# Performance work log

Measured on AMD Instinct MI355X. Metric: run time of the kernel, lower is better.

The kernel has to match this reference:

```python
import jax, jax.numpy as jnp
import numpy as np

TEMPERATURE = 0.5


def setup_inputs() -> dict:
    key = jax.random.key(0)
    ks = jax.random.split(key, 12)
    B, N, T = 128, 64, 256
    IN, H, OUT = N + T, 256, 128
    E = N * (N - 1) // 2  # 2016 upper-tri edges per graph
    total_edges = B * E
    inp = {
        "x_topology": jax.random.normal(ks[0], (B, N, N), jnp.float32),
        "x_temporal": jax.random.normal(ks[1], (B, N, T), jnp.float32),
        "gumbel_u": jax.random.uniform(ks[2], (total_edges,), jnp.float32, 1e-6, 1.0),
        # GNNLayer linear
        "W_gnn": jax.random.normal(ks[3], (IN, H), jnp.float32) / np.sqrt(IN),
        "b_gnn": jnp.zeros((H,), jnp.float32),
        # edge heads (input dim 2*H)
        "W_mean": jax.random.normal(ks[4], (2 * H, OUT), jnp.float32) / np.sqrt(2 * H),
        "b_mean": jnp.zeros((OUT,), jnp.float32),
        "W_var": jax.random.normal(ks[5], (2 * H, OUT), jnp.float32) / np.sqrt(2 * H),
        "b_var": jnp.zeros((OUT,), jnp.float32),
        "W_w": jax.random.normal(ks[6], (2 * H, 1), jnp.float32) / np.sqrt(2 * H),
        "b_w": jnp.zeros((1,), jnp.float32),
    }
    return inp


def reference(x_topology, x_temporal, gumbel_u, W_gnn, b_gnn,
              W_mean, b_mean, W_var, b_var, W_w, b_w):
    B, N, _ = x_topology.shape
    T = x_temporal.shape[-1]
    # Upper-triangular fully-connected edge index (no self loops), batched with node offsets.
    row, col = jnp.triu_indices(N, k=1)          # [E]
    E = row.shape[0]
    offs = (jnp.arange(B) * N)[:, None]          # [B,1]
    src = (row[None, :] + offs).reshape(-1)       # [B*E]
    dst = (col[None, :] + offs).reshape(-1)       # [B*E]

    # Node features: concat topology + temporal, flatten batch of graphs.
    x = jnp.concatenate([x_topology, x_temporal], axis=-1).reshape(B * N, N + T)

    # Mean aggregation (PyG aggr='mean'): messages x[src] scattered to dst; 0 for isolated nodes.
    msg_sum = jax.ops.segment_sum(x[src], dst, num_segments=B * N)      # [B*N, N+T]
    cnt = jax.ops.segment_sum(jnp.ones_like(src, x.dtype), dst, num_segments=B * N)
    agg = jnp.where(cnt[:, None] > 0, msg_sum / jnp.maximum(cnt, 1.0)[:, None], 0.0)

    h = jax.nn.relu(agg @ W_gnn + b_gnn)          # [B*N, H]

    # Edge MLP heads on gathered [src||dst] embeddings.
    ef = jnp.concatenate([h[src], h[dst]], axis=-1)        # [B*E, 2H]
    mean = ef @ W_mean + b_mean                             # [B*E, OUT]
    variance = jax.nn.softplus(ef @ W_var + b_var) + 1e-6   # [B*E, OUT]
    weight = jax.nn.sigmoid((ef @ W_w + b_w)[:, 0])          # [B*E]

    # Gumbel-softmax over the flattened edge-weight vector (dim=-1 of a 1-D tensor).
    g = -jnp.log(-jnp.log(gumbel_u))
    gumbel_w = jax.nn.softmax((weight + g) / TEMPERATURE, axis=-1)

    # Gaussian similarity per edge, scatter into dense adjacency.
    sim = jnp.exp(-0.5 * jnp.mean(mean ** 2 / (variance + 1e-8), axis=-1))
    edge_w = sim * gumbel_w                                  # [B*E]

    b_idx = jnp.repeat(jnp.arange(B), E)
    adj = jnp.zeros((B, N, N), x.dtype).at[b_idx, jnp.tile(row, B), jnp.tile(col, B)].set(edge_w)
    return adj
```

## Files before the change

kernel.cpp:

```cpp
#include <hip/hip_runtime.h>
#include <hip/hip_bf16.h>
#include <math.h>

#define Bg   128
#define Nn   64
#define Tt   256
#define INF  320
#define Hd   256
#define OUTD 128
#define Ee   2016
#define TOTE (Bg*Ee)
#define SCOLS 576
#define MROWS 8192

typedef __attribute__((ext_vector_type(8))) short bf16x8;
typedef __attribute__((ext_vector_type(4))) float f32x4;

static __device__ __forceinline__ ushort f2bf(float v) {
    __hip_bfloat16 h = __float2bfloat16(v);
    return *(ushort*)&h;
}
static __device__ __forceinline__ unsigned fkey(float x) {
    unsigned b = __float_as_uint(x);
    return (b & 0x80000000u) ? ~b : (b | 0x80000000u);
}
static __device__ __forceinline__ float fkeyinv(unsigned k) {
    unsigned b = (k & 0x80000000u) ? (k ^ 0x80000000u) : ~k;
    return __uint_as_float(b);
}

#define CVT_N (INF * Hd)
#define PACK_N (Hd * SCOLS)
__global__ void k_prep(const float* __restrict__ Wg, const float* __restrict__ Wm,
                       const float* __restrict__ Wv, const float* __restrict__ Ww,
                       const float* __restrict__ bm, const float* __restrict__ bv,
                       const float* __restrict__ bw,
                       ushort* __restrict__ Wgb, ushort* __restrict__ Wcat,
                       float* __restrict__ ebias, unsigned* __restrict__ red) {
    int idx = blockIdx.x * 256 + threadIdx.x;
    if (idx == 0) { red[0] = 0u; red[1] = 0u; }
    if (idx < CVT_N) {
        Wgb[idx] = f2bf(Wg[idx]);
        return;
    }
    idx -= CVT_N;
    if (idx < PACK_N) {
        int k = idx / SCOLS, col = idx - k * SCOLS;
        float v = 0.f;
        if (col < 128)       v = Wm[k * 128 + col];
        else if (col < 256)  v = Wm[(256 + k) * 128 + (col - 128)];
        else if (col < 384)  v = Wv[k * 128 + (col - 256)];
        else if (col < 512)  v = Wv[(256 + k) * 128 + (col - 384)];
        else if (col == 512) v = Ww[k];
        else if (col == 513) v = Ww[256 + k];
        Wcat[idx] = f2bf(v);
        return;
    }
    idx -= PACK_N;
    if (idx >= SCOLS) return;
    float e = 0.f;
    if (idx < 128)                    e = bm[idx];
    else if (idx >= 256 && idx < 384) e = bv[idx - 256];
    else if (idx == 512)              e = bw[0];
    ebias[idx] = e;
}

__global__ __launch_bounds__(256) void k_agg(const float* __restrict__ topo,
                                             const float* __restrict__ temp,
                                             ushort* __restrict__ agg) {
    __shared__ float Ltr[64][5];
    int b = blockIdx.x;
    int w = threadIdx.x >> 6, lane = threadIdx.x & 63;
    int f = blockIdx.y * 4 + w;
    float x = (f < Nn) ? topo[(size_t)(b * Nn + lane) * Nn + f]
                       : temp[(size_t)(b * Nn + lane) * Tt + (f - Nn)];
    float incl = x;
    #pragma unroll
    for (int o = 1; o < 64; o <<= 1) {
        float t = __shfl_up(incl, o);
        if (lane >= o) incl += t;
    }
    float excl = incl - x;
    Ltr[lane][w] = lane ? excl / (float)lane : 0.f;
    __syncthreads();
    int node = threadIdx.x >> 2, fi = threadIdx.x & 3;
    agg[(size_t)(b * Nn + node) * INF + blockIdx.y * 4 + fi] = f2bf(Ltr[node][fi]);
}

__global__ __launch_bounds__(256) void k_gemm_mfma(const ushort* __restrict__ A,
                                                   const ushort* __restrict__ B,
                                                   const float* __restrict__ bias,
                                                   ushort* __restrict__ Cb,
                                                   float* __restrict__ Cf,
                                                   int N, int K, int relu, int transC) {
    __shared__ ushort Asl[64 * 32];
    __shared__ ushort Bsl[64 * 32];
    const int tid = threadIdx.x;
    const int w = tid >> 6, lane = tid & 63;
    const int quad = lane >> 4, r16 = lane & 15;
    const int m0 = blockIdx.y * 64, n0 = blockIdx.x * 64;
    const int arow = tid >> 2, aseg = tid & 3;
    const int bk = tid >> 3, bseg = tid & 7;
    f32x4 acc0 = {0,0,0,0}, acc1 = {0,0,0,0}, acc2 = {0,0,0,0}, acc3 = {0,0,0,0};

    for (int k0 = 0; k0 < K; k0 += 32) {
        uint4 av = *(const uint4*)(A + (size_t)(m0 + arow) * K + k0 + aseg * 8);
        *(uint4*)(Asl + arow * 32 + aseg * 8) = av;
        int bcol = n0 + bseg * 8;
        uint4 bvv = *(const uint4*)(B + (size_t)(k0 + bk) * N + bcol);
        ushort tmp[8];
        *(uint4*)tmp = bvv;
        #pragma unroll
        for (int t = 0; t < 8; ++t) Bsl[(bseg * 8 + t) * 32 + bk] = tmp[t];
        __syncthreads();

        bf16x8 af = *(const bf16x8*)(Asl + (w * 16 + r16) * 32 + quad * 8);
        bf16x8 bf0 = *(const bf16x8*)(Bsl + (0 * 16 + r16) * 32 + quad * 8);
        bf16x8 bf1 = *(const bf16x8*)(Bsl + (1 * 16 + r16) * 32 + quad * 8);
        bf16x8 bf2 = *(const bf16x8*)(Bsl + (2 * 16 + r16) * 32 + quad * 8);
        bf16x8 bf3 = *(const bf16x8*)(Bsl + (3 * 16 + r16) * 32 + quad * 8);
        acc0 = __builtin_amdgcn_mfma_f32_16x16x32_bf16(af, bf0, acc0, 0, 0, 0);
        acc1 = __builtin_amdgcn_mfma_f32_16x16x32_bf16(af, bf1, acc1, 0, 0, 0);
        acc2 = __builtin_amdgcn_mfma_f32_16x16x32_bf16(af, bf2, acc2, 0, 0, 0);
        acc3 = __builtin_amdgcn_mfma_f32_16x16x32_bf16(af, bf3, acc3, 0, 0, 0);
        __syncthreads();
    }

    const int row0 = m0 + w * 16 + quad * 4;
    #pragma unroll
    for (int ns = 0; ns < 4; ++ns) {
        f32x4 a = (ns == 0) ? acc0 : (ns == 1) ? acc1 : (ns == 2) ? acc2 : acc3;
        int col = n0 + ns * 16 + r16;
        float bb = bias ? bias[col] : 0.f;
        float vv[4];
        #pragma unroll
        for (int i = 0; i < 4; ++i) {
            float v = a[i] + bb;
            if (relu) v = fmaxf(v, 0.f);
            vv[i] = v;
        }
        if (transC) {
            *(float4*)(Cf + (size_t)col * MROWS + row0) = make_float4(vv[0], vv[1], vv[2], vv[3]);
        } else {
            #pragma unroll
            for (int i = 0; i < 4; ++i) {
                int row = row0 + i;
                if (Cb) Cb[(size_t)row * N + col] = f2bf(vv[i]);
                else    Cf[(size_t)row * N + col] = vv[i];
            }
        }
    }
}

static __device__ __forceinline__ float eterm(float pm, float qm, float pv, float qv) {
    float m = pm + qm;
    float x = pv + qv;
    float sp = fmaxf(x, 0.f) + __logf(1.f + __expf(-fabsf(x)));
    return m * m * __builtin_amdgcn_rcpf(sp + 1.01e-6f);
}

__global__ __launch_bounds__(256) void k_edge4(const float* __restrict__ ST,
                                               const float* __restrict__ gu,
                                               float* __restrict__ sim,
                                               float* __restrict__ lgt,
                                               unsigned* __restrict__ red) {
    __shared__ float L[4][16][132];
    __shared__ float sm[256];
    const int p = blockIdx.x % 10, b = blockIdx.x / 10;
    const int G0v[10] = {0,0,0,0,1,1,1,2,2,3};
    const int G1v[10] = {0,1,2,3,1,2,3,2,3,3};
    const int g0 = G0v[p], g1 = G1v[p];
    const int tid = threadIdx.x;

    #pragma unroll
    for (int rep = 0; rep < 8; ++rep) {
        int it = tid + 256 * rep;
        int arr = it >> 9;
        int c = (it >> 2) & 127, nq = it & 3;
        int g = (arr & 1) ? g1 : g0;
        float4 v = *(const float4*)&ST[(size_t)(arr * 128 + c) * MROWS + b * 64 + g * 16 + nq * 4];
        L[arr][nq * 4 + 0][c] = v.x;
        L[arr][nq * 4 + 1][c] = v.y;
        L[arr][nq * 4 + 2][c] = v.z;
        L[arr][nq * 4 + 3][c] = v.w;
    }
    __syncthreads();

    const int i = tid >> 4, j = tid & 15;
    float acc = 0.f;
    #pragma unroll 4
    for (int t = 0; t < 128; t += 4) {
        float4 mi = *(const float4*)&L[0][i][t];
        float4 mj = *(const float4*)&L[1][j][t];
        float4 vi = *(const float4*)&L[2][i][t];
        float4 vj = *(const float4*)&L[3][j][t];
        acc += eterm(mi.x, mj.x, vi.x, vj.x);
        acc += eterm(mi.y, mj.y, vi.y, vj.y);
        acc += eterm(mi.z, mj.z, vi.z, vj.z);
        acc += eterm(mi.w, mj.w, vi.w, vj.w);
    }

    const int ni = g0 * 16 + i, nj = g1 * 16 + j;
    float lv = -INFINITY;
    if (ni < nj) {
        int e = b * Ee + (ni * (127 - ni)) / 2 + (nj - ni - 1);
        float se = __expf(acc * (-1.f / 256.f));
        float wr = ST[(size_t)512 * MROWS + b * 64 + ni]
                 + ST[(size_t)513 * MROWS + b * 64 + nj];
        float w  = __builtin_amdgcn_rcpf(1.f + __expf(-wr));
        float g  = -__logf(-__logf(gu[e]));
        lv = (w + g) * 2.0f;
        sim[e] = se;
        lgt[e] = lv;
    }
    sm[tid] = lv; __syncthreads();
    for (int s = 128; s; s >>= 1) {
        if (tid < s) sm[tid] = fmaxf(sm[tid], sm[tid + s]);
        __syncthreads();
    }
    if (!tid) atomicMax(&red[0], fkey(sm[0]));
}

__global__ void k_red2(const float* __restrict__ lgt, unsigned* __restrict__ red) {
    __shared__ float sm[256];
    float M = fkeyinv(red[0]);
    float a = 0.f;
    for (int i = blockIdx.x * 256 + threadIdx.x; i < TOTE; i += 256 * 256)
        a += __expf(lgt[i] - M);
    sm[threadIdx.x] = a; __syncthreads();
    for (int s = 128; s; s >>= 1) {
        if (threadIdx.x < s) sm[threadIdx.x] += sm[threadIdx.x + s];
        __syncthreads();
    }
    if (!threadIdx.x) atomicAdd((float*)&red[1], sm[0]);
}

__global__ void k_out(const float* __restrict__ sim, const float* __restrict__ lgt,
                      const unsigned* __restrict__ red, float* __restrict__ out) {
    int idx = blockIdx.x * 256 + threadIdx.x;
    if (idx >= Bg * Nn * Nn) return;
    int b = idx >> 12;
    int rem = idx & 4095;
    int r = rem >> 6, c = rem & 63;
    float v = 0.f;
    if (c > r) {
        int e = b * Ee + (r * (127 - r)) / 2 + (c - r - 1);
        float M = fkeyinv(red[0]);
        float Sinv = __builtin_amdgcn_rcpf(__uint_as_float(red[1]));
        v = sim[e] * __expf(lgt[e] - M) * Sinv;
    }
    out[idx] = v;
}

extern "C" void kernel_launch(void* const* d_in, const int* in_sizes, int n_in,
                              void* d_out, int out_size, void* d_ws, size_t ws_size,
                              hipStream_t stream) {
    const float* topo = (const float*)d_in[0];
    const float* temp = (const float*)d_in[1];
    const float* gu   = (const float*)d_in[2];
    const float* Wg   = (const float*)d_in[3];
    const float* bg   = (const float*)d_in[4];
    const float* Wm   = (const float*)d_in[5];
    const float* bm   = (const float*)d_in[6];
    const float* Wv   = (const float*)d_in[7];
    const float* bv   = (const float*)d_in[8];
    const float* Ww   = (const float*)d_in[9];
    const float* bw   = (const float*)d_in[10];
    float* out = (float*)d_out;

    char* ws = (char*)d_ws;
    size_t off = 0;
    auto carve = [&](size_t bytes) { char* p = ws + off; off = (off + bytes + 255) & ~(size_t)255; return p; };

    char*   r1    = carve((size_t)SCOLS * MROWS * 4);
    float*  ST    = (float*)r1;
    ushort* aggb  = (ushort*)r1;
    ushort* hb    = (ushort*)carve((size_t)MROWS * Hd * 2);
    ushort* Wgb   = (ushort*)carve((size_t)INF * Hd * 2);
    ushort* Wcatb = (ushort*)carve((size_t)Hd * SCOLS * 2);
    float*  ebias = (float*)carve((size_t)SCOLS * 4);
    float*  sim   = (float*)carve((size_t)TOTE * 4);
    float*  lgt   = (float*)carve((size_t)TOTE * 4);
    unsigned* red = (unsigned*)carve(256);

    k_prep<<<(CVT_N + PACK_N + SCOLS + 255) / 256, 256, 0, stream>>>(
        Wg, Wm, Wv, Ww, bm, bv, bw, Wgb, Wcatb, ebias, red);
    k_agg<<<dim3(Bg, INF / 4), 256, 0, stream>>>(topo, temp, aggb);
    k_gemm_mfma<<<dim3(Hd / 64, MROWS / 64), 256, 0, stream>>>(
        aggb, Wgb, bg, hb, nullptr, Hd, INF, 1, 0);
    k_gemm_mfma<<<dim3(SCOLS / 64, MROWS / 64), 256, 0, stream>>>(
        hb, Wcatb, ebias, nullptr, ST, SCOLS, Hd, 0, 1);
    k_edge4<<<Bg * 10, 256, 0, stream>>>(ST, gu, sim, lgt, red);
    k_red2<<<256, 256, 0, stream>>>(lgt, red);
    k_out<<<(Bg * Nn * Nn + 255) / 256, 256, 0, stream>>>(sim, lgt, red, out);
}
```

Before: 162.0 us.

## Drop softmax max pass, transpose weights for GEMM, and batch aggregation tiles

Removes the max-reduction and the separate sum-reduction kernel. The edge kernel now computes exp of the logits directly, writes a single numerator buffer and atomically accumulates the denominator. Weights are stored pre-transposed so GEMM tiles load both operands with vector loads and a K=64 step, replacing scalar transposing LDS stores. The aggregation kernel handles 64 features per block via an LDS tile, with vectorized writes. Skipping the max subtraction relies on the logits being bounded, which risks overflow only for inputs outside that range.

Result: faster. 146.9 us (-9.3%).

```diff
diff --git a/kernel.cpp b/kernel.cpp
--- a/kernel.cpp
+++ b/kernel.cpp
@@ -20,14 +20,6 @@
     __hip_bfloat16 h = __float2bfloat16(v);
     return *(ushort*)&h;
 }
-static __device__ __forceinline__ unsigned fkey(float x) {
-    unsigned b = __float_as_uint(x);
-    return (b & 0x80000000u) ? ~b : (b | 0x80000000u);
-}
-static __device__ __forceinline__ float fkeyinv(unsigned k) {
-    unsigned b = (k & 0x80000000u) ? (k ^ 0x80000000u) : ~k;
-    return __uint_as_float(b);
-}
 
 #define CVT_N (INF * Hd)
 #define PACK_N (Hd * SCOLS)
@@ -35,25 +27,26 @@
                        const float* __restrict__ Wv, const float* __restrict__ Ww,
                        const float* __restrict__ bm, const float* __restrict__ bv,
                        const float* __restrict__ bw,
-                       ushort* __restrict__ Wgb, ushort* __restrict__ Wcat,
+                       ushort* __restrict__ WgbT, ushort* __restrict__ WcatT,
                        float* __restrict__ ebias, unsigned* __restrict__ red) {
     int idx = blockIdx.x * 256 + threadIdx.x;
     if (idx == 0) { red[0] = 0u; red[1] = 0u; }
     if (idx < CVT_N) {
-        Wgb[idx] = f2bf(Wg[idx]);
+        int n = idx / INF, k = idx - n * INF;
+        WgbT[idx] = f2bf(Wg[k * Hd + n]);
         return;
     }
     idx -= CVT_N;
     if (idx < PACK_N) {
-        int k = idx / SCOLS, col = idx - k * SCOLS;
+        int n = idx / Hd, k = idx - n * Hd;
         float v = 0.f;
-        if (col < 128)       v = Wm[k * 128 + col];
-        else if (col < 256)  v = Wm[(256 + k) * 128 + (col - 128)];
-        else if (col < 384)  v = Wv[k * 128 + (col - 256)];
-        else if (col < 512)  v = Wv[(256 + k) * 128 + (col - 384)];
-        else if (col == 512) v = Ww[k];
-        else if (col == 513) v = Ww[256 + k];
-        Wcat[idx] = f2bf(v);
+        if (n < 128)       v = Wm[k * 128 + n];
+        else if (n < 256)  v = Wm[(256 + k) * 128 + (n - 128)];
+        else if (n < 384)  v = Wv[k * 128 + (n - 256)];
+        else if (n < 512)  v = Wv[(256 + k) * 128 + (n - 384)];
+        else if (n == 512) v = Ww[k];
+        else if (n == 513) v = Ww[256 + k];
+        WcatT[idx] = f2bf(v);
         return;
     }
     idx -= PACK_N;
@@ -68,68 +61,87 @@
 __global__ __launch_bounds__(256) void k_agg(const float* __restrict__ topo,
                                              const float* __restrict__ temp,
                                              ushort* __restrict__ agg) {
-    __shared__ float Ltr[64][5];
-    int b = blockIdx.x;
-    int w = threadIdx.x >> 6, lane = threadIdx.x & 63;
-    int f = blockIdx.y * 4 + w;
-    float x = (f < Nn) ? topo[(size_t)(b * Nn + lane) * Nn + f]
-                       : temp[(size_t)(b * Nn + lane) * Tt + (f - Nn)];
-    float incl = x;
-    #pragma unroll
-    for (int o = 1; o < 64; o <<= 1) {
-        float t = __shfl_up(incl, o);
-        if (lane >= o) incl += t;
-    }
-    float excl = incl - x;
-    Ltr[lane][w] = lane ? excl / (float)lane : 0.f;
+    __shared__ float T[64 * 65];
+    const int b = blockIdx.x, ft = blockIdx.y;
+    const int tid = threadIdx.x;
+    const int row = tid >> 2, seg = tid & 3;
+    const float* src = (ft == 0) ? (topo + (size_t)(b * Nn + row) * Nn)
+                                 : (temp + (size_t)(b * Nn + row) * Tt + (ft - 1) * 64);
+    #pragma unroll
+    for (int i = 0; i < 4; ++i) {
+        float4 v = *(const float4*)(src + seg * 16 + i * 4);
+        float* d = &T[row * 65 + seg * 16 + i * 4];
+        d[0] = v.x; d[1] = v.y; d[2] = v.z; d[3] = v.w;
+    }
     __syncthreads();
-    int node = threadIdx.x >> 2, fi = threadIdx.x & 3;
-    agg[(size_t)(b * Nn + node) * INF + blockIdx.y * 4 + fi] = f2bf(Ltr[node][fi]);
+    const int w = tid >> 6, lane = tid & 63;
+    #pragma unroll
+    for (int k = 0; k < 16; ++k) {
+        int f = w * 16 + k;
+        float x = T[lane * 65 + f];
+        float incl = x;
+        #pragma unroll
+        for (int o = 1; o < 64; o <<= 1) {
+            float t = __shfl_up(incl, o);
+            if (lane >= o) incl += t;
+        }
+        float excl = incl - x;
+        T[lane * 65 + f] = lane ? excl * __builtin_amdgcn_rcpf((float)lane) : 0.f;
+    }
+    __syncthreads();
+    const int node = tid >> 2, f0 = (tid & 3) * 16;
+    ushort tmp[16];
+    #pragma unroll
+    for (int i = 0; i < 16; ++i) tmp[i] = f2bf(T[node * 65 + f0 + i]);
+    ushort* dst = agg + (size_t)(b * Nn + node) * INF + ft * 64 + f0;
+    *(uint4*)dst = *(uint4*)tmp;
+    *(uint4*)(dst + 8) = *(uint4*)(tmp + 8);
 }
 
 __global__ __launch_bounds__(256) void k_gemm_mfma(const ushort* __restrict__ A,
-                                                   const ushort* __restrict__ B,
+                                                   const ushort* __restrict__ BT,
                                                    const float* __restrict__ bias,
                                                    ushort* __restrict__ Cb,
                                                    float* __restrict__ Cf,
                                                    int N, int K, int relu, int transC) {
-    __shared__ ushort Asl[64 * 32];
-    __shared__ ushort Bsl[64 * 32];
+    __shared__ ushort Asl[64 * 72];
+    __shared__ ushort Bsl[64 * 72];
     const int tid = threadIdx.x;
     const int w = tid >> 6, lane = tid & 63;
     const int quad = lane >> 4, r16 = lane & 15;
     const int m0 = blockIdx.y * 64, n0 = blockIdx.x * 64;
-    const int arow = tid >> 2, aseg = tid & 3;
-    const int bk = tid >> 3, bseg = tid & 7;
-    f32x4 acc0 = {0,0,0,0}, acc1 = {0,0,0,0}, acc2 = {0,0,0,0}, acc3 = {0,0,0,0};
-
-    for (int k0 = 0; k0 < K; k0 += 32) {
-        uint4 av = *(const uint4*)(A + (size_t)(m0 + arow) * K + k0 + aseg * 8);
-        *(uint4*)(Asl + arow * 32 + aseg * 8) = av;
-        int bcol = n0 + bseg * 8;
-        uint4 bvv = *(const uint4*)(B + (size_t)(k0 + bk) * N + bcol);
-        ushort tmp[8];
-        *(uint4*)tmp = bvv;
+    const int row = tid >> 2, seg = tid & 3;
+    f32x4 acc[4] = {};
+
+    for (int k0 = 0; k0 < K; k0 += 64) {
+        const ushort* ap = A + (size_t)(m0 + row) * K + k0 + seg * 16;
+        uint4 a0 = ((const uint4*)ap)[0];
+        uint4 a1 = ((const uint4*)ap)[1];
+        *(uint4*)(Asl + row * 72 + seg * 16)     = a0;
+        *(uint4*)(Asl + row * 72 + seg * 16 + 8) = a1;
+        const ushort* bp = BT + (size_t)(n0 + row) * K + k0 + seg * 16;
+        uint4 b0 = ((const uint4*)bp)[0];
+        uint4 b1 = ((const uint4*)bp)[1];
+        *(uint4*)(Bsl + row * 72 + seg * 16)     = b0;
+        *(uint4*)(Bsl + row * 72 + seg * 16 + 8) = b1;
+        __syncthreads();
+
+        bf16x8 af0 = *(const bf16x8*)(Asl + (w * 16 + r16) * 72 + quad * 8);
+        bf16x8 af1 = *(const bf16x8*)(Asl + (w * 16 + r16) * 72 + 32 + quad * 8);
         #pragma unroll
-        for (int t = 0; t < 8; ++t) Bsl[(bseg * 8 + t) * 32 + bk] = tmp[t];
+        for (int ns = 0; ns < 4; ++ns) {
+            bf16x8 bf0 = *(const bf16x8*)(Bsl + (ns * 16 + r16) * 72 + quad * 8);
+            bf16x8 bf1 = *(const bf16x8*)(Bsl + (ns * 16 + r16) * 72 + 32 + quad * 8);
+            acc[ns] = __builtin_amdgcn_mfma_f32_16x16x32_bf16(af0, bf0, acc[ns], 0, 0, 0);
+            acc[ns] = __builtin_amdgcn_mfma_f32_16x16x32_bf16(af1, bf1, acc[ns], 0, 0, 0);
+        }
         __syncthreads();
-
-        bf16x8 af = *(const bf16x8*)(Asl + (w * 16 + r16) * 32 + quad * 8);
-        bf16x8 bf0 = *(const bf16x8*)(Bsl + (0 * 16 + r16) * 32 + quad * 8);
-        bf16x8 bf1 = *(const bf16x8*)(Bsl + (1 * 16 + r16) * 32 + quad * 8);
-        bf16x8 bf2 = *(const bf16x8*)(Bsl + (2 * 16 + r16) * 32 + quad * 8);
-        bf16x8 bf3 = *(const bf16x8*)(Bsl + (3 * 16 + r16) * 32 + quad * 8);
-        acc0 = __builtin_amdgcn_mfma_f32_16x16x32_bf16(af, bf0, acc0, 0, 0, 0);
-        acc1 = __builtin_amdgcn_mfma_f32_16x16x32_bf16(af, bf1, acc1, 0, 0, 0);
-        acc2 = __builtin_amdgcn_mfma_f32_16x16x32_bf16(af, bf2, acc2, 0, 0, 0);
-        acc3 = __builtin_amdgcn_mfma_f32_16x16x32_bf16(af, bf3, acc3, 0, 0, 0);
-        __syncthreads();
     }
 
     const int row0 = m0 + w * 16 + quad * 4;
     #pragma unroll
     for (int ns = 0; ns < 4; ++ns) {
-        f32x4 a = (ns == 0) ? acc0 : (ns == 1) ? acc1 : (ns == 2) ? acc2 : acc3;
+        f32x4 a = acc[ns];
         int col = n0 + ns * 16 + r16;
         float bb = bias ? bias[col] : 0.f;
         float vv[4];
@@ -144,9 +156,9 @@
         } else {
             #pragma unroll
             for (int i = 0; i < 4; ++i) {
-                int row = row0 + i;
-                if (Cb) Cb[(size_t)row * N + col] = f2bf(vv[i]);
-                else    Cf[(size_t)row * N + col] = vv[i];
+                int row2 = row0 + i;
+                if (Cb) Cb[(size_t)row2 * N + col] = f2bf(vv[i]);
+                else    Cf[(size_t)row2 * N + col] = vv[i];
             }
         }
     }
@@ -161,8 +173,7 @@
 
 __global__ __launch_bounds__(256) void k_edge4(const float* __restrict__ ST,
                                                const float* __restrict__ gu,
-                                               float* __restrict__ sim,
-                                               float* __restrict__ lgt,
+                                               float* __restrict__ numer,
                                                unsigned* __restrict__ red) {
     __shared__ float L[4][16][132];
     __shared__ float sm[256];
@@ -201,7 +212,7 @@
     }
 
     const int ni = g0 * 16 + i, nj = g1 * 16 + j;
-    float lv = -INFINITY;
+    float en = 0.f;
     if (ni < nj) {
         int e = b * Ee + (ni * (127 - ni)) / 2 + (nj - ni - 1);
         float se = __expf(acc * (-1.f / 256.f));
@@ -209,34 +220,19 @@
                  + ST[(size_t)513 * MROWS + b * 64 + nj];
         float w  = __builtin_amdgcn_rcpf(1.f + __expf(-wr));
         float g  = -__logf(-__logf(gu[e]));
-        lv = (w + g) * 2.0f;
-        sim[e] = se;
-        lgt[e] = lv;
-    }
-    sm[tid] = lv; __syncthreads();
+        en = __expf((w + g) * 2.0f);
+        numer[e] = se * en;
+    }
+    sm[tid] = en; __syncthreads();
     for (int s = 128; s; s >>= 1) {
-        if (tid < s) sm[tid] = fmaxf(sm[tid], sm[tid + s]);
+        if (tid < s) sm[tid] += sm[tid + s];
         __syncthreads();
     }
-    if (!tid) atomicMax(&red[0], fkey(sm[0]));
-}
-
-__global__ void k_red2(const float* __restrict__ lgt, unsigned* __restrict__ red) {
-    __shared__ float sm[256];
-    float M = fkeyinv(red[0]);
-    float a = 0.f;
-    for (int i = blockIdx.x * 256 + threadIdx.x; i < TOTE; i += 256 * 256)
-        a += __expf(lgt[i] - M);
-    sm[threadIdx.x] = a; __syncthreads();
-    for (int s = 128; s; s >>= 1) {
-        if (threadIdx.x < s) sm[threadIdx.x] += sm[threadIdx.x + s];
-        __syncthreads();
-    }
-    if (!threadIdx.x) atomicAdd((float*)&red[1], sm[0]);
-}
-
-__global__ void k_out(const float* __restrict__ sim, const float* __restrict__ lgt,
-                      const unsigned* __restrict__ red, float* __restrict__ out) {
+    if (!tid) atomicAdd((float*)&red[1], sm[0]);
+}
+
+__global__ void k_out(const float* __restrict__ numer, const unsigned* __restrict__ red,
+                      float* __restrict__ out) {
     int idx = blockIdx.x * 256 + threadIdx.x;
     if (idx >= Bg * Nn * Nn) return;
     int b = idx >> 12;
@@ -245,9 +241,8 @@
     float v = 0.f;
     if (c > r) {
         int e = b * Ee + (r * (127 - r)) / 2 + (c - r - 1);
-        float M = fkeyinv(red[0]);
-        float Sinv = __builtin_amdgcn_rcpf(__uint_as_float(red[1]));
-        v = sim[e] * __expf(lgt[e] - M) * Sinv;
+        float Sinv = __builtin_amdgcn_rcpf(((const float*)red)[1]);
+        v = numer[e] * Sinv;
     }
     out[idx] = v;
 }
@@ -276,21 +271,19 @@
     float*  ST    = (float*)r1;
     ushort* aggb  = (ushort*)r1;
     ushort* hb    = (ushort*)carve((size_t)MROWS * Hd * 2);
-    ushort* Wgb   = (ushort*)carve((size_t)INF * Hd * 2);
-    ushort* Wcatb = (ushort*)carve((size_t)Hd * SCOLS * 2);
+    ushort* WgbT  = (ushort*)carve((size_t)INF * Hd * 2);
+    ushort* WcatT = (ushort*)carve((size_t)Hd * SCOLS * 2);
     float*  ebias = (float*)carve((size_t)SCOLS * 4);
-    float*  sim   = (float*)carve((size_t)TOTE * 4);
-    float*  lgt   = (float*)carve((size_t)TOTE * 4);
+    float*  numer = (float*)carve((size_t)TOTE * 4);
     unsigned* red = (unsigned*)carve(256);
 
     k_prep<<<(CVT_N + PACK_N + SCOLS + 255) / 256, 256, 0, stream>>>(
-        Wg, Wm, Wv, Ww, bm, bv, bw, Wgb, Wcatb, ebias, red);
-    k_agg<<<dim3(Bg, INF / 4), 256, 0, stream>>>(topo, temp, aggb);
+        Wg, Wm, Wv, Ww, bm, bv, bw, WgbT, WcatT, ebias, red);
+    k_agg<<<dim3(Bg, INF / 64), 256, 0, stream>>>(topo, temp, aggb);
     k_gemm_mfma<<<dim3(Hd / 64, MROWS / 64), 256, 0, stream>>>(
-        aggb, Wgb, bg, hb, nullptr, Hd, INF, 1, 0);
+        aggb, WgbT, bg, hb, nullptr, Hd, INF, 1, 0);
     k_gemm_mfma<<<dim3(SCOLS / 64, MROWS / 64), 256, 0, stream>>>(
-        hb, Wcatb, ebias, nullptr, ST, SCOLS, Hd, 0, 1);
-    k_edge4<<<Bg * 10, 256, 0, stream>>>(ST, gu, sim, lgt, red);
-    k_red2<<<256, 256, 0, stream>>>(lgt, red);
-    k_out<<<(Bg * Nn * Nn + 255) / 256, 256, 0, stream>>>(sim, lgt, red, out);
-}
+        hb, WcatT, ebias, nullptr, ST, SCOLS, Hd, 0, 1);
+    k_edge4<<<Bg * 10, 256, 0, stream>>>(ST, gu, numer, red);
+    k_out<<<(Bg * Nn * Nn + 255) / 256, 256, 0, stream>>>(numer, red, out);
+}
```
